# Kernel optimization log

Measured on AMD Instinct MI355X. Metric: run time of the kernel, lower is better.

The kernel has to match this reference:

```python
import jax, jax.numpy as jnp
import numpy as np

GAMMA = 0.9
SCALE_BASE = 512.0


def _xpos(x, downscale=False):
    """XPOS rotary embedding (torchscale variant) applied to x: (B, L, D)."""
    B, L, D = x.shape
    half = D // 2
    # per-channel magnitude base: ((2i) + 0.4*D) / (1.4*D), i over even channels
    scale_vec = (jnp.arange(0, D, 2, dtype=jnp.float32) + 0.4 * D) / (1.4 * D)  # (half,)
    power = jnp.arange(L, dtype=jnp.float32) / SCALE_BASE                        # (L,)
    scale = scale_vec[None, :] ** power[:, None]                                 # (L, half)
    if downscale:
        scale = 1.0 / scale
    # fixed sinusoidal frequencies over `half` dims
    inv_freq = 1.0 / (10000.0 ** (jnp.arange(half, dtype=jnp.float32) / half))   # (half,)
    sinusoid = jnp.arange(L, dtype=jnp.float32)[:, None] * inv_freq[None, :]     # (L, half)
    sin = jnp.repeat(jnp.sin(sinusoid) * scale, 2, axis=-1)                      # (L, D) interleaved dup
    cos = jnp.repeat(jnp.cos(sinusoid) * scale, 2, axis=-1)
    # rotate_every_two: (x0,x1,x2,x3,...) -> (-x1,x0,-x3,x2,...)
    x_even = x[..., 0::2]
    x_odd = x[..., 1::2]
    rot = jnp.stack((-x_odd, x_even), axis=-1).reshape(x.shape)
    return x * cos + rot * sin


def _get_D(seq_len):
    n = jnp.arange(seq_len, dtype=jnp.float32)[:, None]
    m = jnp.arange(seq_len, dtype=jnp.float32)[None, :]
    D = GAMMA ** jnp.abs(n - m)  # non-causal decay, no NaNs since gamma > 0
    return D


def setup_inputs() -> dict:
    key = jax.random.key(0)
    k1, k2, k3, k4 = jax.random.split(key, 4)
    B, L, H, Dh = 8, 2048, 1024, 1024
    X = jax.random.normal(k1, (B, L, H), dtype=jnp.float32)
    W_Q = jax.random.normal(k2, (H, Dh), dtype=jnp.float32) / H
    W_K = jax.random.normal(k3, (H, Dh), dtype=jnp.float32) / H
    W_V = jax.random.normal(k4, (H, Dh), dtype=jnp.float32) / H
    return {"X": X, "W_Q": W_Q, "W_K": W_K, "W_V": W_V}


def reference(X, W_Q, W_K, W_V):
    B, L, H = X.shape
    D = _get_D(L)                       # (L, L)
    Q = _xpos(X @ W_Q)                  # (B, L, Dh)
    K = _xpos(X @ W_K, downscale=True)  # (B, L, Dh)
    V = X @ W_V                         # (B, L, Dv)
    scores = jnp.einsum('bqd,bkd->bqk', Q, K)   # (B, L, L)
    p_attn = jax.nn.softmax(scores, axis=-1)
    p_attn = p_attn * D[None, :, :]              # elementwise decay AFTER softmax
    return jnp.einsum('bqk,bkv->bqv', p_attn, V)
```

## Files before the change

### kernel.cpp

```cpp
#include <hip/hip_runtime.h>
#include <math.h>


#define LDIM 2048
#define HDIM 1024
#define MTOT 16384

typedef unsigned short u16;
typedef unsigned int u32;
typedef __attribute__((ext_vector_type(16))) float f32x16;
typedef __attribute__((ext_vector_type(8))) short s16x8;

#define GLD16(gp, lp) __builtin_amdgcn_global_load_lds( \
    (const __attribute__((address_space(1))) void*)(gp), \
    (__attribute__((address_space(3))) void*)(lp), 16, 0, 0)

__device__ __forceinline__ u16 f2bf(float f) {
    unsigned u = __float_as_uint(f);
    return (u16)((u + 0x7FFFu + ((u >> 16) & 1u)) >> 16);
}

__device__ __forceinline__ void sincos_rev(float ang, float* sn, float* cs) {
    double dr = (double)ang * 0.15915494309189535;
    dr -= __builtin_floor(dr);
    float fr = (float)dr;
    float s_, c_;
    asm("v_sin_f32 %0, %1" : "=v"(s_) : "v"(fr));
    asm("v_cos_f32 %0, %1" : "=v"(c_) : "v"(fr));
    *sn = s_; *cs = c_;
}

#define ROW32(reg, laneHi) (((reg) & 3) + 8 * ((reg) >> 2) + 4 * (laneHi))

__device__ __forceinline__ void gemm256(const u16* __restrict__ A,
                                        const u16* __restrict__ B,
                                        int lda, int ldb, int K, int m0, int n0,
                                        char* smem, int tid, f32x16 (*acc)[2])
{
    const int wv = tid >> 6, ln = tid & 63;
    const int wm = wv >> 2, wn = wv & 3;
    const int lane31 = ln & 31, laneHi = ln >> 5;
    const int srow = tid >> 3;
    const int scol = ((tid & 7) ^ (srow & 7)) * 8;

    const u16* ap[4];
    const u16* bp[4];
#pragma unroll
    for (int r = 0; r < 4; ++r) {
        ap[r] = A + (size_t)(m0 + r * 64 + srow) * lda + scol;
        bp[r] = B + (size_t)(n0 + r * 64 + srow) * ldb + scol;
    }

    int abyte[4], bbyte[2];
    const int slot_r = (laneHi ^ (lane31 & 7)) << 4;
#pragma unroll
    for (int fm = 0; fm < 4; ++fm)
        abyte[fm] = (wm * 128 + fm * 32 + lane31) * 128 + slot_r;
#pragma unroll
    for (int fn = 0; fn < 2; ++fn)
        bbyte[fn] = 32768 + (wn * 64 + fn * 32 + lane31) * 128 + slot_r;

#define STAGE256(sl) do {                                                  \
        char* d_ = smem + (sl) * 65536;                                    \
        _Pragma("unroll")                                                  \
        for (int r_ = 0; r_ < 4; ++r_) {                                   \
            GLD16(ap[r_], d_ + r_ * 8192 + tid * 16);                      \
            ap[r_] += 64;                                                  \
        }                                                                  \
        _Pragma("unroll")                                                  \
        for (int r_ = 0; r_ < 4; ++r_) {                                   \
            GLD16(bp[r_], d_ + 32768 + r_ * 8192 + tid * 16);              \
            bp[r_] += 64;                                                  \
        }                                                                  \
    } while (0)

    const int nk = K >> 6;
    STAGE256(0);
    __syncthreads();

    int buf = 0;
#pragma unroll 1
    for (int t = 0; t < nk; ++t) {
        if (t + 1 < nk) STAGE256(buf ^ 1);
        const char* Bb = smem + buf * 65536;
#pragma unroll
        for (int ks = 0; ks < 4; ++ks) {
            s16x8 af[4], bf[2];
#pragma unroll
            for (int fm = 0; fm < 4; ++fm)
                af[fm] = *(const s16x8*)(Bb + (abyte[fm] ^ (ks << 5)));
#pragma unroll
            for (int fn = 0; fn < 2; ++fn)
                bf[fn] = *(const s16x8*)(Bb + (bbyte[fn] ^ (ks << 5)));
#pragma unroll
            for (int fm = 0; fm < 4; ++fm)
#pragma unroll
                for (int fn = 0; fn < 2; ++fn)
                    acc[fm][fn] = __builtin_amdgcn_mfma_f32_32x32x16_bf16(
                        af[fm], bf[fn], acc[fm][fn], 0, 0, 0);
        }
        __syncthreads();
        buf ^= 1;
    }
#undef STAGE256
}

__global__ __launch_bounds__(256) void prep_all(
    const float* __restrict__ X,
    const float* __restrict__ Wq, const float* __restrict__ Wk,
    const float* __restrict__ Wv,
    u16* __restrict__ Xb, u16* __restrict__ WT,
    u32* __restrict__ CSq, u32* __restrict__ CSk)
{
    __shared__ float L[64][65];
    const int bid = blockIdx.x;
    if (bid < 2048) {
        const int n4 = MTOT * HDIM / 4;
        int i = bid * 256 + threadIdx.x;
        const int stride = 2048 * 256;
        for (; i < n4; i += stride) {
            float4 v = ((const float4*)X)[i];
            ushort4 o = make_ushort4(f2bf(v.x), f2bf(v.y), f2bf(v.z), f2bf(v.w));
            ((ushort4*)Xb)[i] = o;
        }
    } else if (bid < 4096) {
        const int l = bid - 2048;
        for (int ih = threadIdx.x; ih < 512; ih += 256) {
            float invf = exp2f(-13.287712379549449f * (1.f / 512.f) * (float)ih);
            float sn, cs;
            sincos_rev((float)l * invf, &sn, &cs);
            float l2sv = log2f(((float)(2 * ih) + 409.6f) * (1.f / 1433.6f));
            float e = (float)l * (1.f / 512.f) * l2sv;
            float sq = exp2f(e), sk = exp2f(-e);
            CSq[l * 512 + ih] = (u32)f2bf(cs * sq) | ((u32)f2bf(sn * sq) << 16);
            CSk[l * 512 + ih] = (u32)f2bf(cs * sk) | ((u32)f2bf(sn * sk) << 16);
        }
    } else {
        const int r = bid - 4096;
        const int z = r >> 8;
        const int y = (r >> 4) & 15;
        const int x = r & 15;
        const float* Wz = (z == 0) ? Wq : (z == 1) ? Wk : Wv;
        u16* Oz = WT + (size_t)z * HDIM * HDIM;
        const int k0 = y * 64, n0 = x * 64;
        const int t = threadIdx.x;
        const int r_ = t >> 4, c4 = (t & 15) * 4;
#pragma unroll
        for (int it = 0; it < 4; ++it) {
            const int row = it * 16 + r_;
            float4 v = *(const float4*)&Wz[(size_t)(k0 + row) * HDIM + n0 + c4];
            L[row][c4 + 0] = v.x; L[row][c4 + 1] = v.y;
            L[row][c4 + 2] = v.z; L[row][c4 + 3] = v.w;
        }
        __syncthreads();
#pragma unroll
        for (int it = 0; it < 4; ++it) {
            const int orow = it * 16 + r_;
            ushort4 o = make_ushort4(f2bf(L[c4 + 0][orow]), f2bf(L[c4 + 1][orow]),
                                     f2bf(L[c4 + 2][orow]), f2bf(L[c4 + 3][orow]));
            *(ushort4*)&Oz[(size_t)(n0 + orow) * HDIM + k0 + c4] = o;
        }
    }
}

__global__ __launch_bounds__(512, 2) void qkv_gemm(
    const u16* __restrict__ Xb, const u16* __restrict__ WT,
    const u32* __restrict__ CSq, const u32* __restrict__ CSk,
    u16* __restrict__ Qb, u16* __restrict__ Kb, u16* __restrict__ Vt)
{
    __shared__ __align__(16) char smem[256 * 264 * 2];
    const int bid = blockIdx.x;
    const int xcd = bid & 7, t = bid >> 3;
    const int m8 = t & 7;
    const int n_ = (t >> 3) & 3;
    const int z  = t >> 5;
    const int m0 = (xcd * 8 + m8) * 256;
    const int n0 = n_ * 256;
    const int tid = threadIdx.x;

    f32x16 acc[4][2] = {};

    gemm256(Xb, WT + (size_t)z * HDIM * HDIM, HDIM, HDIM, HDIM, m0, n0, smem, tid, acc);

    const int wv = tid >> 6, ln = tid & 63;
    const int wm = wv >> 2, wn = wv & 3;
    const int lane31 = ln & 31, laneHi = ln >> 5;
    const int l0 = m0 & (LDIM - 1);
    u16* T = (u16*)smem;

    if (z < 2) {
        const u32* CS = (z == 0) ? CSq : CSk;
#pragma unroll
        for (int fn = 0; fn < 2; ++fn) {
            const int gc = n0 + wn * 64 + fn * 32 + lane31;
            const int ih = gc >> 1;
            const float sgn = (gc & 1) ? 1.f : -1.f;
            const u32* tb = CS + (size_t)l0 * 512 + ih;
#pragma unroll
            for (int fm = 0; fm < 4; ++fm) {
#pragma unroll
                for (int reg = 0; reg < 16; ++reg) {
                    const int rowl = wm * 128 + fm * 32 + ROW32(reg, laneHi);
                    u32 v = tb[(size_t)rowl * 512];
                    float cs = __uint_as_float(v << 16);
                    float sn = __uint_as_float(v & 0xFFFF0000u);
                    float c = acc[fm][fn][reg];
                    float p = __shfl_xor(c, 1);
                    T[rowl * 264 + wn * 64 + fn * 32 + lane31] =
                        f2bf(c * cs + sgn * p * sn);
                }
            }
        }
        __syncthreads();
        u16* Out = (z == 0) ? Qb : Kb;
        const int row_ = tid >> 5, slot = tid & 31;
#pragma unroll
        for (int g = 0; g < 16; ++g) {
            const int row = g * 16 + row_;
            s16x8 v = *(const s16x8*)&T[row * 264 + slot * 8];
            *(s16x8*)&Out[(size_t)(m0 + row) * HDIM + n0 + slot * 8] = v;
        }
    } else {
#pragma unroll
        for (int fn = 0; fn < 2; ++fn)
#pragma unroll
            for (int fm = 0; fm < 4; ++fm)
#pragma unroll
                for (int reg = 0; reg < 16; ++reg)
                    T[(wn * 64 + fn * 32 + lane31) * 264 +
                      wm * 128 + fm * 32 + ROW32(reg, laneHi)] =
                        f2bf(acc[fm][fn][reg]);
        __syncthreads();
        const int b = m0 >> 11;
        const int row_ = tid >> 5, slot = tid & 31;
#pragma unroll
        for (int g = 0; g < 16; ++g) {
            const int row = g * 16 + row_;
            s16x8 v = *(const s16x8*)&T[row * 264 + slot * 8];
            *(s16x8*)&Vt[((size_t)b * HDIM + n0 + row) * LDIM + l0 + slot * 8] = v;
        }
    }
}

__global__ __launch_bounds__(512, 2) void qk_gemm(
    const u16* __restrict__ Q, const u16* __restrict__ Km,
    u16* __restrict__ Wm, float* __restrict__ Zp)
{
    __shared__ __align__(16) char smem[256 * 264 * 2];
    __shared__ float Zl[4][256];
    const int bid = blockIdx.x;
    const int b = bid & 7, t = bid >> 3;
    const int mt = t & 7;
    const int nt = t >> 3;
    const int m0 = mt * 256;
    const int n0 = nt * 256;
    const int tid = threadIdx.x;

    f32x16 acc[4][2] = {};

    gemm256(Q + (size_t)b * LDIM * HDIM, Km + (size_t)b * LDIM * HDIM,
            HDIM, HDIM, HDIM, m0, n0, smem, tid, acc);

    const int wv = tid >> 6, ln = tid & 63;
    const int wm = wv >> 2, wn = wv & 3;
    const int lane31 = ln & 31, laneHi = ln >> 5;
    u16* T = (u16*)smem;
    const float LOG2E = 1.4426950408889634f;
    const float LOG2G = -0.15200309344504997f;

#pragma unroll
    for (int fm = 0; fm < 4; ++fm) {
        float ps[16];
#pragma unroll
        for (int reg = 0; reg < 16; ++reg) ps[reg] = 0.f;
#pragma unroll
        for (int fn = 0; fn < 2; ++fn) {
            const int gk = n0 + wn * 64 + fn * 32 + lane31;
#pragma unroll
            for (int reg = 0; reg < 16; ++reg) {
                const int mloc = wm * 128 + fm * 32 + ROW32(reg, laneHi);
                const int gq = m0 + mloc;
                float t1 = acc[fm][fn][reg] * LOG2E;
                float e = exp2f(t1);
                int dd = gq - gk; dd = dd < 0 ? -dd : dd;
                ps[reg] += e;
                T[mloc * 264 + wn * 64 + fn * 32 + lane31] =
                    f2bf(exp2f(t1 + (float)dd * LOG2G));
            }
        }
#pragma unroll
        for (int reg = 0; reg < 16; ++reg) {
            float s = ps[reg];
            s += __shfl_xor(s, 1); s += __shfl_xor(s, 2);
            s += __shfl_xor(s, 4); s += __shfl_xor(s, 8);
            s += __shfl_xor(s, 16);
            if (lane31 == 0)
                Zl[wn][wm * 128 + fm * 32 + ROW32(reg, laneHi)] = s;
        }
    }
    __syncthreads();

    const int row_ = tid >> 5, slot = tid & 31;
#pragma unroll
    for (int g = 0; g < 16; ++g) {
        const int row = g * 16 + row_;
        s16x8 v = *(const s16x8*)&T[row * 264 + slot * 8];
        *(s16x8*)&Wm[((size_t)b * LDIM + m0 + row) * LDIM + n0 + slot * 8] = v;
    }
    if (tid < 256)
        Zp[((size_t)b * 8 + nt) * LDIM + m0 + tid] =
            Zl[0][tid] + Zl[1][tid] + Zl[2][tid] + Zl[3][tid];
}

__global__ __launch_bounds__(512, 2) void pv_gemm(
    const u16* __restrict__ Wm, const u16* __restrict__ Vt,
    const float* __restrict__ Zp, float* __restrict__ Out)
{
    __shared__ __align__(16) char smem[2 * 65536];
    __shared__ float Zinv[256];
    const int bid = blockIdx.x;
    const int b = bid & 7, t = bid >> 3;
    const int mt4 = t & 3;
    const int nt = (t >> 2) & 3;
    const int mtH = t >> 4;
    const int m0 = (mtH * 4 + mt4) * 256;
    const int n0 = nt * 256;
    const int tid = threadIdx.x;

    if (tid < 256) {
        float zz = 0.f;
#pragma unroll
        for (int nb = 0; nb < 8; ++nb)
            zz += Zp[((size_t)b * 8 + nb) * LDIM + m0 + tid];
        Zinv[tid] = 1.0f / zz;
    }

    f32x16 acc[4][2] = {};

    gemm256(Wm + (size_t)b * LDIM * LDIM, Vt + (size_t)b * HDIM * LDIM,
            LDIM, LDIM, LDIM, m0, n0, smem, tid, acc);

    const int wv = tid >> 6, ln = tid & 63;
    const int wm = wv >> 2, wn = wv & 3;
    const int lane31 = ln & 31, laneHi = ln >> 5;
    float* Ob = Out + (size_t)b * LDIM * HDIM;
#pragma unroll
    for (int fm = 0; fm < 4; ++fm)
#pragma unroll
        for (int fn = 0; fn < 2; ++fn) {
            const int gn = n0 + wn * 64 + fn * 32 + lane31;
#pragma unroll
            for (int reg = 0; reg < 16; ++reg) {
                const int row = wm * 128 + fm * 32 + ROW32(reg, laneHi);
                Ob[(size_t)(m0 + row) * HDIM + gn] = acc[fm][fn][reg] * Zinv[row];
            }
        }
}

extern "C" void kernel_launch(void* const* d_in, const int* in_sizes, int n_in,
                              void* d_out, int out_size, void* d_ws, size_t ws_size,
                              hipStream_t stream)
{
    (void)in_sizes; (void)n_in; (void)out_size; (void)ws_size;
    const float* X  = (const float*)d_in[0];
    const float* Wq = (const float*)d_in[1];
    const float* Wk = (const float*)d_in[2];
    const float* Wv = (const float*)d_in[3];
    char* ws = (char*)d_ws;
    const size_t MB = 1024 * 1024;

    u16* Wmat = (u16*)ws;
    u16* Xb   = (u16*)ws;
    u16* WT   = (u16*)(ws + 32 * MB);
    u16* Qb   = (u16*)(ws + 64 * MB);
    u16* Kb   = (u16*)(ws + 96 * MB);
    u16* Vt   = (u16*)(ws + 128 * MB);
    float* Zp = (float*)(ws + 160 * MB);
    u32* CSq  = (u32*)(ws + 161 * MB);
    u32* CSk  = (u32*)(ws + 165 * MB);

    prep_all<<<4864, 256, 0, stream>>>(X, Wq, Wk, Wv, Xb, WT, CSq, CSk);
    qkv_gemm<<<768, 512, 0, stream>>>(Xb, WT, CSq, CSk, Qb, Kb, Vt);
    qk_gemm<<<512, 512, 0, stream>>>(Qb, Kb, Wmat, Zp);
    pv_gemm<<<256, 512, 0, stream>>>(Wmat, Vt, Zp, (float*)d_out);
}
```

Before: 323.1 us.

## Interleave staged global-to-LDS loads with MFMA phases using fine-grained barriers

```diff
diff --git a/kernel.cpp b/kernel.cpp
--- a/kernel.cpp
+++ b/kernel.cpp
@@ -60,49 +60,55 @@
     for (int fn = 0; fn < 2; ++fn)
         bbyte[fn] = 32768 + (wn * 64 + fn * 32 + lane31) * 128 + slot_r;
 
-#define STAGE256(sl) do {                                                  \
-        char* d_ = smem + (sl) * 65536;                                    \
-        _Pragma("unroll")                                                  \
-        for (int r_ = 0; r_ < 4; ++r_) {                                   \
-            GLD16(ap[r_], d_ + r_ * 8192 + tid * 16);                      \
-            ap[r_] += 64;                                                  \
-        }                                                                  \
-        _Pragma("unroll")                                                  \
-        for (int r_ = 0; r_ < 4; ++r_) {                                   \
-            GLD16(bp[r_], d_ + 32768 + r_ * 8192 + tid * 16);              \
-            bp[r_] += 64;                                                  \
-        }                                                                  \
+#define SGA0(e_) do{ char* d_=smem+(e_)*65536+tid*16;       GLD16(ap[0],d_); GLD16(ap[1],d_+8192); ap[0]+=64; ap[1]+=64; }while(0)
+#define SGA1(e_) do{ char* d_=smem+(e_)*65536+16384+tid*16; GLD16(ap[2],d_); GLD16(ap[3],d_+8192); ap[2]+=64; ap[3]+=64; }while(0)
+#define SGB0(e_) do{ char* d_=smem+(e_)*65536+32768+tid*16; GLD16(bp[0],d_); GLD16(bp[1],d_+8192); bp[0]+=64; bp[1]+=64; }while(0)
+#define SGB1(e_) do{ char* d_=smem+(e_)*65536+49152+tid*16; GLD16(bp[2],d_); GLD16(bp[3],d_+8192); bp[2]+=64; bp[3]+=64; }while(0)
+
+#define READS(Bb_, ks) do {                                                   \
+        _Pragma("unroll") for (int fm_ = 0; fm_ < 4; ++fm_)                   \
+            af[fm_] = *(const s16x8*)((Bb_) + (abyte[fm_] ^ ((ks) << 5)));    \
+        _Pragma("unroll") for (int fn_ = 0; fn_ < 2; ++fn_)                   \
+            bf[fn_] = *(const s16x8*)((Bb_) + (bbyte[fn_] ^ ((ks) << 5)));    \
     } while (0)
 
+#define MFMA8 do { __builtin_amdgcn_s_setprio(1);                             \
+        _Pragma("unroll") for (int fm_ = 0; fm_ < 4; ++fm_)                   \
+            _Pragma("unroll") for (int fn_ = 0; fn_ < 2; ++fn_)               \
+                acc[fm_][fn_] = __builtin_amdgcn_mfma_f32_32x32x16_bf16(      \
+                    af[fm_], bf[fn_], acc[fm_][fn_], 0, 0, 0);                \
+        __builtin_amdgcn_s_setprio(0); } while (0)
+
+#define BAR do { __builtin_amdgcn_s_barrier();                                \
+                 __builtin_amdgcn_sched_barrier(0); } while (0)
+
     const int nk = K >> 6;
-    STAGE256(0);
-    __syncthreads();
-
-    int buf = 0;
+
+    SGA0(0); SGB0(0); SGA1(0); SGB1(0);
+
 #pragma unroll 1
     for (int t = 0; t < nk; ++t) {
-        if (t + 1 < nk) STAGE256(buf ^ 1);
-        const char* Bb = smem + buf * 65536;
-#pragma unroll
-        for (int ks = 0; ks < 4; ++ks) {
-            s16x8 af[4], bf[2];
-#pragma unroll
-            for (int fm = 0; fm < 4; ++fm)
-                af[fm] = *(const s16x8*)(Bb + (abyte[fm] ^ (ks << 5)));
-#pragma unroll
-            for (int fn = 0; fn < 2; ++fn)
-                bf[fn] = *(const s16x8*)(Bb + (bbyte[fn] ^ (ks << 5)));
-#pragma unroll
-            for (int fm = 0; fm < 4; ++fm)
-#pragma unroll
-                for (int fn = 0; fn < 2; ++fn)
-                    acc[fm][fn] = __builtin_amdgcn_mfma_f32_32x32x16_bf16(
-                        af[fm], bf[fn], acc[fm][fn], 0, 0, 0);
-        }
-        __syncthreads();
-        buf ^= 1;
-    }
-#undef STAGE256
+        const int d = t & 1, e = d ^ 1;
+        const bool pre = (t + 1 < nk);
+        const char* Bb = smem + d * 65536;
+        s16x8 af[4], bf[2];
+
+        if (pre) { SGA0(e); asm volatile("s_waitcnt vmcnt(2)" ::: "memory"); }
+        else     {          asm volatile("s_waitcnt vmcnt(0)" ::: "memory"); }
+        BAR;
+        READS(Bb, 0); if (pre) SGB0(e); BAR; MFMA8; BAR;
+        READS(Bb, 1); if (pre) SGA1(e); BAR; MFMA8; BAR;
+        READS(Bb, 2); if (pre) SGB1(e); BAR; MFMA8; BAR;
+        READS(Bb, 3);                   BAR; MFMA8; BAR;
+    }
+    __syncthreads();
+#undef SGA0
+#undef SGA1
+#undef SGB0
+#undef SGB1
+#undef READS
+#undef MFMA8
+#undef BAR
 }
 
 __global__ __launch_bounds__(256) void prep_all(
@@ -334,6 +340,7 @@
             zz += Zp[((size_t)b * 8 + nb) * LDIM + m0 + tid];
         Zinv[tid] = 1.0f / zz;
     }
+    __syncthreads();
 
     f32x16 acc[4][2] = {};
 
```

Result: slower. 334.3 us (+3.5%).
